# Kernel tuning notes

Hardware: AMD Instinct MI355X
Metric: run time of the kernel (lower is better)

The kernel has to match this reference:

```python
import jax, jax.numpy as jnp
import numpy as np

B, N, D, H = 2, 2048, 1024, 16
HD = D // H
SCALE = HD ** -0.5


def setup_inputs() -> dict:
    key = jax.random.key(0)
    ks = jax.random.split(key, 9)
    s = D ** -0.5
    return {
        "x": jax.random.normal(ks[0], (B, N, D), dtype=jnp.float32),
        "Wq": jax.random.normal(ks[1], (D, D), dtype=jnp.float32) * s,
        "bq": jax.random.normal(ks[2], (D,), dtype=jnp.float32) * 0.01,
        "Wk": jax.random.normal(ks[3], (D, D), dtype=jnp.float32) * s,
        "bk": jax.random.normal(ks[4], (D,), dtype=jnp.float32) * 0.01,
        "Wv": jax.random.normal(ks[5], (D, D), dtype=jnp.float32) * s,
        "bv": jax.random.normal(ks[6], (D,), dtype=jnp.float32) * 0.01,
        "Wo": jax.random.normal(ks[7], (D, D), dtype=jnp.float32) * s,
        "bo": jax.random.normal(ks[8], (D,), dtype=jnp.float32) * 0.01,
    }


def reference(x, Wq, bq, Wk, bk, Wv, bv, Wo, bo):
    # Q/K/V projections (torch Linear: x @ W.T + b), split into heads: (B,H,N,HD)
    def proj(W, b):
        return (x @ W.T + b).reshape(B, N, H, HD).transpose(0, 2, 1, 3)

    q = proj(Wq, bq)
    k = proj(Wk, bk)
    v = proj(Wv, bv)
    # Scaled dot-product attention with explicit (B,H,N,N) scores
    scores = jnp.einsum("bhnd,bhmd->bhnm", q, k) * SCALE
    attn = jax.nn.softmax(scores, axis=-1)
    y = jnp.einsum("bhnm,bhmd->bhnd", attn, v)
    y = y.transpose(0, 2, 1, 3).reshape(B, N, D)
    # Output projection
    return y @ Wo.T + bo
```

## Files before the change

### kernel.cpp

```cpp
#include <hip/hip_runtime.h>

#define BB 2
#define NN 2048
#define DD 1024
#define HH 16
#define HD 64
#define SCALE 0.125f

typedef unsigned short u16;
typedef unsigned int u32;
typedef __attribute__((ext_vector_type(4))) short short4v;
typedef __attribute__((ext_vector_type(8))) short short8;
typedef __attribute__((ext_vector_type(4))) float float4v;

__device__ __forceinline__ float b2f(u16 u) {
    union { float f; u32 i; } x; x.i = ((u32)u) << 16; return x.f;
}
__device__ __forceinline__ u16 f2b(float f) {
    union { float f; u32 i; } x; x.f = f;
    u32 i = x.i;
    return (u16)((i + 0x7fffu + ((i >> 16) & 1u)) >> 16);
}

#if __has_builtin(__builtin_amdgcn_exp2f)
#define EXP2F(x) __builtin_amdgcn_exp2f(x)
#else
#define EXP2F(x) __expf((x) * 0.69314718055994531f)
#endif

#if __has_builtin(__builtin_amdgcn_rcpf)
#define RCPF(x) __builtin_amdgcn_rcpf(x)
#else
#define RCPF(x) (1.0f / (x))
#endif

__device__ __forceinline__ void gl_lds16(const u16* g, u16* l) {
    __builtin_amdgcn_global_load_lds(
        (__attribute__((address_space(1))) void*)(void*)g,
        (__attribute__((address_space(3))) void*)l, 16, 0, 0);
}

__global__ __launch_bounds__(256) void cvt_all(
    const float* __restrict__ x,
    const float* __restrict__ Wq, const float* __restrict__ Wk,
    const float* __restrict__ Wv, const float* __restrict__ Wo,
    u16* __restrict__ xb, u16* __restrict__ W4)
{
    int e = (blockIdx.x * 256 + threadIdx.x) * 8;
    const float* s;
    u16* d;
    if (e < 4194304) { s = x + e; d = xb + e; }
    else {
        int e2 = e - 4194304;
        int which = e2 >> 20;
        int off = e2 & 1048575;
        s = ((which == 0) ? Wq : (which == 1) ? Wk : (which == 2) ? Wv : Wo) + off;
        d = W4 + e2;
    }
    float4v a = *(const float4v*)s;
    float4v b = *(const float4v*)(s + 4);
    short8 r;
    r[0] = (short)f2b(a[0]); r[1] = (short)f2b(a[1]);
    r[2] = (short)f2b(a[2]); r[3] = (short)f2b(a[3]);
    r[4] = (short)f2b(b[0]); r[5] = (short)f2b(b[1]);
    r[6] = (short)f2b(b[2]); r[7] = (short)f2b(b[3]);
    *(short8*)d = r;
}


__global__ __launch_bounds__(256) void gemm_qkv(
    const u16* __restrict__ xb,
    const u16* __restrict__ Wqb, const float* __restrict__ bq,
    const u16* __restrict__ Wkb, const float* __restrict__ bk,
    const u16* __restrict__ Wvb, const float* __restrict__ bv,
    u16* __restrict__ Qo, u16* __restrict__ Ko, u16* __restrict__ Vt)
{
    const int tm = blockIdx.y;
    const int tn_all = blockIdx.x;
    const int mat = tn_all >> 3;
    const int tn = tn_all & 7;

    const u16* __restrict__ W     = (mat == 0) ? Wqb : (mat == 1) ? Wkb : Wvb;
    const float* __restrict__ bias = (mat == 0) ? bq : (mat == 1) ? bk : bv;

    __shared__ u16 As[2][128 * 32];
    __shared__ u16 Bs[2][128 * 32];

    const int tid  = threadIdx.x;
    const int wave = tid >> 6, lane = tid & 63;
    const int wm = wave >> 1, wn = wave & 1;
    const int quad = lane >> 4, l16 = lane & 15;

    const int r0 = tid >> 2, c0 = tid & 3;
    const int r1 = r0 + 64;

    const u16* ga0 = &xb[(size_t)(tm * 128 + r0) * DD + c0 * 8];
    const u16* ga1 = &xb[(size_t)(tm * 128 + r1) * DD + c0 * 8];
    const u16* gb0 = &W [(size_t)(tn * 128 + r0) * DD + c0 * 8];
    const u16* gb1 = &W [(size_t)(tn * 128 + r1) * DD + c0 * 8];

    float4v acc[4][4] = {};

    gl_lds16(ga0, &As[0][tid * 8]);
    gl_lds16(ga1, &As[0][(256 + tid) * 8]);
    gl_lds16(gb0, &Bs[0][tid * 8]);
    gl_lds16(gb1, &Bs[0][(256 + tid) * 8]);

    int cur = 0;
    for (int k0 = 0; k0 < DD; k0 += 32) {
        __syncthreads();
        const int kn = (k0 + 32) & (DD - 1);
        gl_lds16(ga0 + kn, &As[cur ^ 1][tid * 8]);
        gl_lds16(ga1 + kn, &As[cur ^ 1][(256 + tid) * 8]);
        gl_lds16(gb0 + kn, &Bs[cur ^ 1][tid * 8]);
        gl_lds16(gb1 + kn, &Bs[cur ^ 1][(256 + tid) * 8]);

        short8 af[4], bf[4];
        #pragma unroll
        for (int mi = 0; mi < 4; ++mi)
            af[mi] = *(const short8*)&As[cur][(wm * 64 + mi * 16 + l16) * 32 + quad * 8];
        #pragma unroll
        for (int ni = 0; ni < 4; ++ni)
            bf[ni] = *(const short8*)&Bs[cur][(wn * 64 + ni * 16 + l16) * 32 + quad * 8];

        #pragma unroll
        for (int mi = 0; mi < 4; ++mi)
            #pragma unroll
            for (int ni = 0; ni < 4; ++ni)
                acc[mi][ni] = __builtin_amdgcn_mfma_f32_16x16x32_bf16(
                    af[mi], bf[ni], acc[mi][ni], 0, 0, 0);
        cur ^= 1;
    }
    asm volatile("s_waitcnt vmcnt(0)" ::: "memory");

    #pragma unroll
    for (int mi = 0; mi < 4; ++mi) {
        #pragma unroll
        for (int ni = 0; ni < 4; ++ni) {
            int cc = tn * 128 + wn * 64 + ni * 16 + l16;
            int h = cc >> 6, hd = cc & 63;
            float bv_ = bias[cc];
            if (mat == 2) {
                short4v v4;
                #pragma unroll
                for (int rr = 0; rr < 4; ++rr)
                    v4[rr] = (short)f2b(acc[mi][ni][rr] + bv_);
                int R0 = tm * 128 + wm * 64 + mi * 16 + quad * 4;
                int b = R0 >> 11, n = R0 & 2047;
                *(short4v*)&Vt[(((size_t)(b * HH + h)) * HD + hd) * NN + n] = v4;
            } else {
                u16* Out = (mat == 0) ? Qo : Ko;
                #pragma unroll
                for (int rr = 0; rr < 4; ++rr) {
                    int R = tm * 128 + wm * 64 + mi * 16 + quad * 4 + rr;
                    int b = R >> 11, n = R & 2047;
                    Out[(((size_t)(b * HH + h)) * NN + n) * HD + hd] =
                        f2b(acc[mi][ni][rr] + bv_);
                }
            }
        }
    }
}

__global__ __launch_bounds__(256) void gemm_out(
    const u16* __restrict__ A, const u16* __restrict__ W,
    const float* __restrict__ bias, float* __restrict__ Out)
{
    const int tm = blockIdx.y;
    const int tn = blockIdx.x;

    __shared__ u16 As[2][64 * 32];
    __shared__ u16 Bs[2][128 * 32];

    const int tid  = threadIdx.x;
    const int wave = tid >> 6, lane = tid & 63;
    const int quad = lane >> 4, l16 = lane & 15;
    const int wn = wave;

    const int r0 = tid >> 2, c0 = tid & 3;

    const u16* ga  = &A[(size_t)(tm * 64 + r0) * DD + c0 * 8];
    const u16* gb0 = &W[(size_t)(tn * 128 + r0) * DD + c0 * 8];
    const u16* gb1 = &W[(size_t)(tn * 128 + r0 + 64) * DD + c0 * 8];

    float4v acc[4][2] = {};

    gl_lds16(ga,  &As[0][tid * 8]);
    gl_lds16(gb0, &Bs[0][tid * 8]);
    gl_lds16(gb1, &Bs[0][(256 + tid) * 8]);

    int cur = 0;
    for (int k0 = 0; k0 < DD; k0 += 32) {
        __syncthreads();
        const int kn = (k0 + 32) & (DD - 1);
        gl_lds16(ga + kn,  &As[cur ^ 1][tid * 8]);
        gl_lds16(gb0 + kn, &Bs[cur ^ 1][tid * 8]);
        gl_lds16(gb1 + kn, &Bs[cur ^ 1][(256 + tid) * 8]);

        short8 af[4], bf[2];
        #pragma unroll
        for (int mi = 0; mi < 4; ++mi)
            af[mi] = *(const short8*)&As[cur][(mi * 16 + l16) * 32 + quad * 8];
        #pragma unroll
        for (int ni = 0; ni < 2; ++ni)
            bf[ni] = *(const short8*)&Bs[cur][(wn * 32 + ni * 16 + l16) * 32 + quad * 8];

        #pragma unroll
        for (int mi = 0; mi < 4; ++mi)
            #pragma unroll
            for (int ni = 0; ni < 2; ++ni)
                acc[mi][ni] = __builtin_amdgcn_mfma_f32_16x16x32_bf16(
                    af[mi], bf[ni], acc[mi][ni], 0, 0, 0);
        cur ^= 1;
    }
    asm volatile("s_waitcnt vmcnt(0)" ::: "memory");

    #pragma unroll
    for (int mi = 0; mi < 4; ++mi) {
        #pragma unroll
        for (int ni = 0; ni < 2; ++ni) {
            int cc = tn * 128 + wn * 32 + ni * 16 + l16;
            float bv_ = bias[cc];
            #pragma unroll
            for (int rr = 0; rr < 4; ++rr) {
                int R = tm * 64 + mi * 16 + quad * 4 + rr;
                Out[(size_t)R * DD + cc] = acc[mi][ni][rr] + bv_;
            }
        }
    }
}

__global__ __launch_bounds__(512) void attn_mfma(
    const u16* __restrict__ Q, const u16* __restrict__ K,
    const u16* __restrict__ Vt, u16* __restrict__ Y)
{
    const int id   = blockIdx.x;
    const int xcd  = id & 7;
    const int slot = id >> 3;
    const int bh   = (xcd << 2) | (slot & 3);
    const int qb   = slot >> 2;

    const int tid  = threadIdx.x;
    const int wave = tid >> 6, lane = tid & 63;
    const int quad = lane >> 4, l16 = lane & 15;

    const u16* __restrict__ Qb = Q + (size_t)bh * NN * HD;
    const u16* __restrict__ Kb = K + (size_t)bh * NN * HD;
    const u16* __restrict__ Vb = Vt + (size_t)bh * HD * NN;

    __shared__ u16 Ks[2][64 * 64];
    __shared__ u16 Vs[2][64 * 64];
    __shared__ u16 Ps[8][16 * 72];

    short8 qa[2];
    {
        int qrow = qb * 128 + wave * 16 + l16;
        #pragma unroll
        for (int kc = 0; kc < 2; ++kc) {
            short8 t = *(const short8*)&Qb[(size_t)qrow * HD + kc * 32 + quad * 8];
            #pragma unroll
            for (int j = 0; j < 8; ++j)
                qa[kc][j] = (short)f2b(b2f((u16)t[j]) * SCALE);
        }
    }

    short8 onesB;
    #pragma unroll
    for (int j = 0; j < 8; ++j) onesB[j] = (short)0x3F80;

    float4v oc[4] = {};
    float4v la = {};

    const int srow = tid >> 3, sslot = tid & 7;
    const int oct = (sslot + srow) & 7;

    const int fs0 = ((quad - l16) & 7) * 8;
    const int fs1 = ((4 + quad - l16) & 7) * 8;

    gl_lds16(&Kb[(size_t)srow * HD + oct * 8], &Ks[0][tid * 8]);
    gl_lds16(&Vb[(size_t)srow * NN + oct * 8], &Vs[0][tid * 8]);

    for (int k0 = 0; k0 < NN; k0 += 64) {
        const int cur = (k0 >> 6) & 1;
        const int kn = (k0 + 64) & (NN - 1);

        __syncthreads();

        gl_lds16(&Kb[(size_t)(kn + srow) * HD + oct * 8], &Ks[cur ^ 1][tid * 8]);
        gl_lds16(&Vb[(size_t)srow * NN + kn + oct * 8],   &Vs[cur ^ 1][tid * 8]);

        float4v sc[4];
        __builtin_amdgcn_s_setprio(1);
        #pragma unroll
        for (int kt = 0; kt < 4; ++kt) {
            short8 kb0 = *(const short8*)&Ks[cur][(kt * 16 + l16) * 64 + fs0];
            short8 kb1 = *(const short8*)&Ks[cur][(kt * 16 + l16) * 64 + fs1];
            float4v z = {};
            z = __builtin_amdgcn_mfma_f32_16x16x32_bf16(qa[0], kb0, z, 0, 0, 0);
            sc[kt] = __builtin_amdgcn_mfma_f32_16x16x32_bf16(qa[1], kb1, z, 0, 0, 0);
        }
        __builtin_amdgcn_s_setprio(0);

        #pragma unroll
        for (int rr = 0; rr < 4; ++rr) {
            #pragma unroll
            for (int kt = 0; kt < 4; ++kt) {
                float p = EXP2F(__builtin_fmaf(sc[kt][rr], 1.44269504f,
                                               -11.5415603f));
                union { float f; u32 i; } px; px.f = p;
                Ps[wave][(quad * 4 + rr) * 72 + kt * 16 + l16] = (u16)(px.i >> 16);
            }
        }
        asm volatile("s_waitcnt lgkmcnt(0)" ::: "memory");

        short8 pa0 = *(const short8*)&Ps[wave][l16 * 72 + quad * 8];
        short8 pa1 = *(const short8*)&Ps[wave][l16 * 72 + 32 + quad * 8];

        __builtin_amdgcn_s_setprio(1);
        la = __builtin_amdgcn_mfma_f32_16x16x32_bf16(pa0, onesB, la, 0, 0, 0);
        la = __builtin_amdgcn_mfma_f32_16x16x32_bf16(pa1, onesB, la, 0, 0, 0);
        #pragma unroll
        for (int ht = 0; ht < 4; ++ht) {
            short8 vb0 = *(const short8*)&Vs[cur][(ht * 16 + l16) * 64 + fs0];
            short8 vb1 = *(const short8*)&Vs[cur][(ht * 16 + l16) * 64 + fs1];
            oc[ht] = __builtin_amdgcn_mfma_f32_16x16x32_bf16(pa0, vb0, oc[ht], 0, 0, 0);
            oc[ht] = __builtin_amdgcn_mfma_f32_16x16x32_bf16(pa1, vb1, oc[ht], 0, 0, 0);
        }
        __builtin_amdgcn_s_setprio(0);
    }
    asm volatile("s_waitcnt vmcnt(0)" ::: "memory");

    const int b = bh >> 4, h = bh & 15;
    float inv[4];
    #pragma unroll
    for (int rr = 0; rr < 4; ++rr) inv[rr] = RCPF(la[rr]);
    #pragma unroll
    for (int ht = 0; ht < 4; ++ht) {
        #pragma unroll
        for (int rr = 0; rr < 4; ++rr) {
            int n = qb * 128 + wave * 16 + quad * 4 + rr;
            int col = h * HD + ht * 16 + l16;
            Y[((size_t)(b * NN + n)) * DD + col] = f2b(oc[ht][rr] * inv[rr]);
        }
    }
}

extern "C" void kernel_launch(void* const* d_in, const int* in_sizes, int n_in,
                              void* d_out, int out_size, void* d_ws, size_t ws_size,
                              hipStream_t stream) {
    const float* x  = (const float*)d_in[0];
    const float* Wq = (const float*)d_in[1];
    const float* bq = (const float*)d_in[2];
    const float* Wk = (const float*)d_in[3];
    const float* bk = (const float*)d_in[4];
    const float* Wv = (const float*)d_in[5];
    const float* bv = (const float*)d_in[6];
    const float* Wo = (const float*)d_in[7];
    const float* bo = (const float*)d_in[8];
    float* out = (float*)d_out;

    const size_t M1 = 1024 * 1024;
    u16* base = (u16*)d_ws;
    u16* xb  = base;
    u16* W4  = base + 4 * M1;
    u16* Wqb = W4;
    u16* Wkb = W4 + 1 * M1;
    u16* Wvb = W4 + 2 * M1;
    u16* Wob = W4 + 3 * M1;
    u16* Qw  = base + 8 * M1;
    u16* Kw  = base + 12 * M1;
    u16* Vtw = base + 16 * M1;
    u16* Yw  = xb;

    cvt_all<<<dim3(4096), 256, 0, stream>>>(x, Wq, Wk, Wv, Wo, xb, W4);

    gemm_qkv<<<dim3(24, 32), 256, 0, stream>>>(xb, Wqb, bq, Wkb, bk, Wvb, bv,
                                               Qw, Kw, Vtw);

    attn_mfma<<<dim3(512), 512, 0, stream>>>(Qw, Kw, Vtw, Yw);

    gemm_out<<<dim3(8, 64), 256, 0, stream>>>(Yw, Wob, bo, out);
}
```

Baseline: 214.8 us.

## Triple-buffer LDS tiles in QKV and output GEMMs with partial vmcnt waits

Both projection GEMMs move from double to triple LDS buffering, keeping two tiles of global-to-LDS loads in flight. A partial s_waitcnt vmcnt plus a raw s_barrier replaces the full __syncthreads, so each wave waits only for the oldest tile. This is meant to hide global load latency behind more MFMA work. The cost is 50% more LDS per block, which may lower occupancy, and correctness now depends on the counted outstanding-load accounting.

```diff
diff --git a/kernel.cpp b/kernel.cpp
--- a/kernel.cpp
+++ b/kernel.cpp
@@ -83,8 +83,8 @@
     const u16* __restrict__ W     = (mat == 0) ? Wqb : (mat == 1) ? Wkb : Wvb;
     const float* __restrict__ bias = (mat == 0) ? bq : (mat == 1) ? bk : bv;
 
-    __shared__ u16 As[2][128 * 32];
-    __shared__ u16 Bs[2][128 * 32];
+    __shared__ u16 As[3][128 * 32];
+    __shared__ u16 Bs[3][128 * 32];
 
     const int tid  = threadIdx.x;
     const int wave = tid >> 6, lane = tid & 63;
@@ -101,27 +101,33 @@
 
     float4v acc[4][4] = {};
 
-    gl_lds16(ga0, &As[0][tid * 8]);
-    gl_lds16(ga1, &As[0][(256 + tid) * 8]);
-    gl_lds16(gb0, &Bs[0][tid * 8]);
-    gl_lds16(gb1, &Bs[0][(256 + tid) * 8]);
-
-    int cur = 0;
-    for (int k0 = 0; k0 < DD; k0 += 32) {
-        __syncthreads();
-        const int kn = (k0 + 32) & (DD - 1);
-        gl_lds16(ga0 + kn, &As[cur ^ 1][tid * 8]);
-        gl_lds16(ga1 + kn, &As[cur ^ 1][(256 + tid) * 8]);
-        gl_lds16(gb0 + kn, &Bs[cur ^ 1][tid * 8]);
-        gl_lds16(gb1 + kn, &Bs[cur ^ 1][(256 + tid) * 8]);
+    gl_lds16(ga0,      &As[0][tid * 8]);
+    gl_lds16(ga1,      &As[0][(256 + tid) * 8]);
+    gl_lds16(gb0,      &Bs[0][tid * 8]);
+    gl_lds16(gb1,      &Bs[0][(256 + tid) * 8]);
+    gl_lds16(ga0 + 32, &As[1][tid * 8]);
+    gl_lds16(ga1 + 32, &As[1][(256 + tid) * 8]);
+    gl_lds16(gb0 + 32, &Bs[1][tid * 8]);
+    gl_lds16(gb1 + 32, &Bs[1][(256 + tid) * 8]);
+
+    int cb = 0, b2 = 2;
+    for (int it = 0; it < 32; ++it) {
+        asm volatile("s_waitcnt vmcnt(4)" ::: "memory");
+        __builtin_amdgcn_s_barrier();
+
+        const int k2 = ((it + 2) & 31) << 5;
+        gl_lds16(ga0 + k2, &As[b2][tid * 8]);
+        gl_lds16(ga1 + k2, &As[b2][(256 + tid) * 8]);
+        gl_lds16(gb0 + k2, &Bs[b2][tid * 8]);
+        gl_lds16(gb1 + k2, &Bs[b2][(256 + tid) * 8]);
 
         short8 af[4], bf[4];
         #pragma unroll
         for (int mi = 0; mi < 4; ++mi)
-            af[mi] = *(const short8*)&As[cur][(wm * 64 + mi * 16 + l16) * 32 + quad * 8];
+            af[mi] = *(const short8*)&As[cb][(wm * 64 + mi * 16 + l16) * 32 + quad * 8];
         #pragma unroll
         for (int ni = 0; ni < 4; ++ni)
-            bf[ni] = *(const short8*)&Bs[cur][(wn * 64 + ni * 16 + l16) * 32 + quad * 8];
+            bf[ni] = *(const short8*)&Bs[cb][(wn * 64 + ni * 16 + l16) * 32 + quad * 8];
 
         #pragma unroll
         for (int mi = 0; mi < 4; ++mi)
@@ -129,7 +135,9 @@
             for (int ni = 0; ni < 4; ++ni)
                 acc[mi][ni] = __builtin_amdgcn_mfma_f32_16x16x32_bf16(
                     af[mi], bf[ni], acc[mi][ni], 0, 0, 0);
-        cur ^= 1;
+
+        cb = (cb == 2) ? 0 : cb + 1;
+        b2 = (b2 == 2) ? 0 : b2 + 1;
     }
     asm volatile("s_waitcnt vmcnt(0)" ::: "memory");
 
@@ -169,8 +177,8 @@
     const int tm = blockIdx.y;
     const int tn = blockIdx.x;
 
-    __shared__ u16 As[2][64 * 32];
-    __shared__ u16 Bs[2][128 * 32];
+    __shared__ u16 As[3][64 * 32];
+    __shared__ u16 Bs[3][128 * 32];
 
     const int tid  = threadIdx.x;
     const int wave = tid >> 6, lane = tid & 63;
@@ -185,25 +193,30 @@
 
     float4v acc[4][2] = {};
 
-    gl_lds16(ga,  &As[0][tid * 8]);
-    gl_lds16(gb0, &Bs[0][tid * 8]);
-    gl_lds16(gb1, &Bs[0][(256 + tid) * 8]);
-
-    int cur = 0;
-    for (int k0 = 0; k0 < DD; k0 += 32) {
-        __syncthreads();
-        const int kn = (k0 + 32) & (DD - 1);
-        gl_lds16(ga + kn,  &As[cur ^ 1][tid * 8]);
-        gl_lds16(gb0 + kn, &Bs[cur ^ 1][tid * 8]);
-        gl_lds16(gb1 + kn, &Bs[cur ^ 1][(256 + tid) * 8]);
+    gl_lds16(ga,       &As[0][tid * 8]);
+    gl_lds16(gb0,      &Bs[0][tid * 8]);
+    gl_lds16(gb1,      &Bs[0][(256 + tid) * 8]);
+    gl_lds16(ga + 32,  &As[1][tid * 8]);
+    gl_lds16(gb0 + 32, &Bs[1][tid * 8]);
+    gl_lds16(gb1 + 32, &Bs[1][(256 + tid) * 8]);
+
+    int cb = 0, b2 = 2;
+    for (int it = 0; it < 32; ++it) {
+        asm volatile("s_waitcnt vmcnt(3)" ::: "memory");
+        __builtin_amdgcn_s_barrier();
+
+        const int k2 = ((it + 2) & 31) << 5;
+        gl_lds16(ga + k2,  &As[b2][tid * 8]);
+        gl_lds16(gb0 + k2, &Bs[b2][tid * 8]);
+        gl_lds16(gb1 + k2, &Bs[b2][(256 + tid) * 8]);
 
         short8 af[4], bf[2];
         #pragma unroll
         for (int mi = 0; mi < 4; ++mi)
-            af[mi] = *(const short8*)&As[cur][(mi * 16 + l16) * 32 + quad * 8];
+            af[mi] = *(const short8*)&As[cb][(mi * 16 + l16) * 32 + quad * 8];
         #pragma unroll
         for (int ni = 0; ni < 2; ++ni)
-            bf[ni] = *(const short8*)&Bs[cur][(wn * 32 + ni * 16 + l16) * 32 + quad * 8];
+            bf[ni] = *(const short8*)&Bs[cb][(wn * 32 + ni * 16 + l16) * 32 + quad * 8];
 
         #pragma unroll
         for (int mi = 0; mi < 4; ++mi)
@@ -211,7 +224,9 @@
             for (int ni = 0; ni < 2; ++ni)
                 acc[mi][ni] = __builtin_amdgcn_mfma_f32_16x16x32_bf16(
                     af[mi], bf[ni], acc[mi][ni], 0, 0, 0);
-        cur ^= 1;
+
+        cb = (cb == 2) ? 0 : cb + 1;
+        b2 = (b2 == 2) ? 0 : b2 + 1;
     }
     asm volatile("s_waitcnt vmcnt(0)" ::: "memory");
 
```

Measured after the change: 216.3 us. Within noise of the previous version (+0.7%).
